# Kernel tuning notes

Hardware: AMD Instinct MI355X
Metric: run time of the kernel (lower is better)

Reference implementation:

```python
import jax, jax.numpy as jnp
import numpy as np

N = 100000
E = 1600000
IN_C, HID, OUT_C = 500, 256, 40
K, ALPHA = 10, 0.1
LN_EPS = 1e-5


def setup_inputs() -> dict:
    key = jax.random.key(0)
    ks = jax.random.split(key, 12)
    glorot = lambda k, i, o: jax.random.normal(k, (i, o), jnp.float32) * (1.0 / np.sqrt(i))
    return {
        "x": jax.random.normal(ks[0], (N, IN_C), jnp.float32),
        "edge_index": jax.random.randint(ks[1], (2, E), 0, N, jnp.int64),
        "W1": glorot(ks[2], IN_C, HID), "b1": jnp.zeros((HID,), jnp.float32),
        "g1": jnp.ones((HID,), jnp.float32), "be1": jnp.zeros((HID,), jnp.float32),
        "W2": glorot(ks[3], HID, HID), "b2": jnp.zeros((HID,), jnp.float32),
        "g2": jnp.ones((HID,), jnp.float32), "be2": jnp.zeros((HID,), jnp.float32),
        "W3": glorot(ks[4], HID, OUT_C), "b3": jnp.zeros((OUT_C,), jnp.float32),
    }


def _layernorm(h, g, b):
    mu = jnp.mean(h, axis=-1, keepdims=True)
    var = jnp.mean(jnp.square(h - mu), axis=-1, keepdims=True)
    return (h - mu) * jax.lax.rsqrt(var + LN_EPS) * g + b


def reference(x, edge_index, W1, b1, g1, be1, W2, b2, g2, be2, W3, b3):
    # --- MLP (eval mode: dropout inactive) ---
    h = _layernorm(jax.nn.gelu(x @ W1 + b1, approximate=False), g1, be1)
    h = _layernorm(jax.nn.gelu(h @ W2 + b2, approximate=False), g2, be2)
    h = h @ W3 + b3  # [N, OUT_C]

    # --- GCN normalization with self-loops (PyG gcn_norm) ---
    loops = jnp.arange(N, dtype=edge_index.dtype)
    row = jnp.concatenate([edge_index[0], loops])  # source
    col = jnp.concatenate([edge_index[1], loops])  # target
    deg = jax.ops.segment_sum(jnp.ones_like(col, jnp.float32), col, num_segments=N)
    dinv = jnp.where(deg > 0, jax.lax.rsqrt(deg), 0.0)
    norm = dinv[row] * dinv[col]  # [E+N]

    # --- APPNP: K steps of h <- (1-alpha) * A_hat h + alpha * h0 ---
    h0 = h
    for _ in range(K):
        msg = norm[:, None] * h[row]                       # gather + scale
        agg = jax.ops.segment_sum(msg, col, num_segments=N)  # scatter-add
        h = (1.0 - ALPHA) * agg + ALPHA * h0
    return h
```

## Files before the change

kernel.cpp:

```cpp
#include <hip/hip_runtime.h>
#include <hip/hip_bf16.h>
#include <math.h>

#define N_NODES 100000
#define N_EDGES 1600000
#define IN_C    500
#define HID     256
#define OUT_C   40
#define K_ITERS 10
#define ALPHA   0.1f
#define LN_EPS  1e-5f

#define K1PAD   512
#define K2PAD   256

#define SCAN_CHUNK 1024
#define NBLK_SCAN  ((N_NODES + SCAN_CHUNK - 1) / SCAN_CHUNK)

typedef __attribute__((ext_vector_type(8))) short bf16x8;
typedef __attribute__((ext_vector_type(4))) float f32x4;

__device__ __forceinline__ void split2(float a, short& hi, short& lo) {
    const unsigned ua = __float_as_uint(a);
    hi = (short)(ua >> 16);
    const float r = a - __uint_as_float(ua & 0xffff0000u);
    lo = (short)(__float_as_uint(r) >> 16);
}

__device__ __forceinline__ void async_load16(const void* g, void* l) {
    __builtin_amdgcn_global_load_lds(
        (const __attribute__((address_space(1))) void*)g,
        (__attribute__((address_space(3))) void*)l, 16, 0, 0);
}

__global__ void deg_count_kernel(const int* __restrict__ col, int* __restrict__ cnt, int e) {
    int i = blockIdx.x * blockDim.x + threadIdx.x;
    if (i < e) atomicAdd(&cnt[col[i]], 1);
}

__global__ void dinv_kernel(const int* __restrict__ cnt, float* __restrict__ dinv, int n) {
    int i = blockIdx.x * blockDim.x + threadIdx.x;
    if (i < n) dinv[i] = rsqrtf((float)cnt[i] + 1.0f);
}

__global__ __launch_bounds__(256) void scan_partial_kernel(const int* __restrict__ cnt,
                                                           int* __restrict__ bsum) {
    __shared__ int s[256];
    const int base = blockIdx.x * SCAN_CHUNK;
    const int t = threadIdx.x;
    int sum = 0;
    #pragma unroll
    for (int j = 0; j < 4; j++) {
        int idx = base + t * 4 + j;
        if (idx < N_NODES) sum += cnt[idx];
    }
    s[t] = sum;
    __syncthreads();
    for (int off = 128; off > 0; off >>= 1) {
        if (t < off) s[t] += s[t + off];
        __syncthreads();
    }
    if (t == 0) bsum[blockIdx.x] = s[0];
}

__global__ __launch_bounds__(128) void scan_bsum_kernel(int* __restrict__ bsum, int nblk) {
    __shared__ int s[128];
    const int t = threadIdx.x;
    const int orig = (t < nblk) ? bsum[t] : 0;
    s[t] = orig;
    __syncthreads();
    for (int off = 1; off < 128; off <<= 1) {
        int v = 0;
        if (t >= off) v = s[t - off];
        __syncthreads();
        s[t] += v;
        __syncthreads();
    }
    if (t < nblk) bsum[t] = s[t] - orig;
}

__global__ __launch_bounds__(256) void scan_final_kernel(const int* __restrict__ cnt,
                                                         const int* __restrict__ bsum,
                                                         int* __restrict__ offs) {
    __shared__ int s[256];
    const int base = blockIdx.x * SCAN_CHUNK;
    const int t = threadIdx.x;
    int v[4];
    int lsum = 0;
    #pragma unroll
    for (int j = 0; j < 4; j++) {
        int idx = base + t * 4 + j;
        v[j] = (idx < N_NODES) ? cnt[idx] : 0;
        lsum += v[j];
    }
    s[t] = lsum;
    __syncthreads();
    const int orig = lsum;
    for (int off = 1; off < 256; off <<= 1) {
        int u = 0;
        if (t >= off) u = s[t - off];
        __syncthreads();
        s[t] += u;
        __syncthreads();
    }
    int run = bsum[blockIdx.x] + (s[t] - orig);
    #pragma unroll
    for (int j = 0; j < 4; j++) {
        int idx = base + t * 4 + j;
        if (idx < N_NODES) offs[idx] = run;
        run += v[j];
    }
}

__global__ void set_total_kernel(int* __restrict__ offs) {
    if (threadIdx.x == 0 && blockIdx.x == 0) offs[N_NODES] = N_EDGES;
}

__global__ void csr_fill_kernel(const int* __restrict__ row, const int* __restrict__ col,
                                const float* __restrict__ dinv, const int* __restrict__ offs,
                                int* __restrict__ cursor, int2* __restrict__ csr_ew, int e) {
    int i = blockIdx.x * blockDim.x + threadIdx.x;
    if (i >= e) return;
    const int r = row[i], c = col[i];
    const int p = offs[c] + atomicAdd(&cursor[c], 1);
    csr_ew[p] = make_int2(r, __float_as_int(dinv[r] * dinv[c]));
}

__global__ __launch_bounds__(256) void wsplit_kernel(
    const float* __restrict__ W, short* __restrict__ hi, short* __restrict__ lo,
    int K, int Nn, int Kpad)
{
    const int idx = blockIdx.x * 256 + threadIdx.x;
    if (idx >= Nn * Kpad) return;
    const int n = idx / Kpad, k = idx - n * Kpad;
    const float v = (k < K) ? W[(size_t)k * Nn + n] : 0.0f;
    short h, l;
    split2(v, h, l);
    hi[idx] = h;
    lo[idx] = l;
}

#define GBM 64
#define GBN 256
#define GBK 32
#define NSTEP1 (K1PAD / GBK)
#define NSTEP2 (K2PAD / GBK)

__global__ __launch_bounds__(256, 2) void gemm1_fused_kernel(
    const float* __restrict__ X,
    const short* __restrict__ Bhi, const short* __restrict__ Blo,
    const float* __restrict__ bias, float* __restrict__ C, int M)
{
    __shared__ short As[2][2][GBM * GBK];
    __shared__ short Bs[2][2][GBN * GBK];

    const int tid  = threadIdx.x;
    const int wid  = tid >> 6, lane = tid & 63;
    const int wm   = wid >> 1, wn = wid & 1;
    const int fm   = lane & 15, fq = lane >> 4;
    const int row0 = blockIdx.x * GBM;

    const int ar   = tid >> 2;
    const int aseg = tid & 3;
    const int gr   = min(row0 + ar, M - 1);
    const int asw  = (aseg ^ ((ar >> 1) & 3)) * 8;

    f32x4 acc[2][8] = {};

    auto stageB = [&](int ks, int buf) {
        const int k0 = ks * GBK;
        #pragma unroll
        for (int i = 0; i < 4; i++) {
            const int c  = i * 256 + tid;
            const int n  = c >> 2;
            const int k8 = ((c & 3) ^ ((n >> 1) & 3)) * 8;
            const int cb = (i * 256 + wid * 64) * 8;
            const size_t oB = (size_t)n * K1PAD + k0 + k8;
            async_load16(Bhi + oB, &Bs[buf][0][cb]);
            async_load16(Blo + oB, &Bs[buf][1][cb]);
        }
    };
    auto loadX = [&](int ks, float* v) {
        const int kb = ks * GBK + aseg * 8;
        if (kb + 8 <= IN_C) {
            const float4 v0 = *(const float4*)(X + (size_t)gr * IN_C + kb);
            const float4 v1 = *(const float4*)(X + (size_t)gr * IN_C + kb + 4);
            v[0]=v0.x; v[1]=v0.y; v[2]=v0.z; v[3]=v0.w;
            v[4]=v1.x; v[5]=v1.y; v[6]=v1.z; v[7]=v1.w;
        } else {
            #pragma unroll
            for (int j = 0; j < 8; j++)
                v[j] = (kb + j < IN_C) ? X[(size_t)gr * IN_C + kb + j] : 0.0f;
        }
    };
    auto writeA = [&](const float* v, int buf) {
        bf16x8 h8, l8;
        #pragma unroll
        for (int j = 0; j < 8; j++) { short th, tl; split2(v[j], th, tl); h8[j] = th; l8[j] = tl; }
        *(bf16x8*)&As[buf][0][ar * GBK + asw] = h8;
        *(bf16x8*)&As[buf][1][ar * GBK + asw] = l8;
    };
    auto compute = [&](int buf) {
        bf16x8 ah[2], al[2];
        #pragma unroll
        for (int tm = 0; tm < 2; tm++) {
            const int r   = wm * 32 + tm * 16 + fm;
            const int ks8 = (fq ^ ((r >> 1) & 3)) * 8;
            ah[tm] = *(const bf16x8*)&As[buf][0][r * GBK + ks8];
            al[tm] = *(const bf16x8*)&As[buf][1][r * GBK + ks8];
        }
        #pragma unroll
        for (int tn = 0; tn < 8; tn++) {
            const int cc  = wn * 128 + tn * 16 + fm;
            const int ks8 = (fq ^ ((cc >> 1) & 3)) * 8;
            const bf16x8 bh = *(const bf16x8*)&Bs[buf][0][cc * GBK + ks8];
            const bf16x8 bl = *(const bf16x8*)&Bs[buf][1][cc * GBK + ks8];
            #pragma unroll
            for (int tm = 0; tm < 2; tm++) {
                acc[tm][tn] = __builtin_amdgcn_mfma_f32_16x16x32_bf16(ah[tm], bh, acc[tm][tn], 0, 0, 0);
                acc[tm][tn] = __builtin_amdgcn_mfma_f32_16x16x32_bf16(ah[tm], bl, acc[tm][tn], 0, 0, 0);
                acc[tm][tn] = __builtin_amdgcn_mfma_f32_16x16x32_bf16(al[tm], bh, acc[tm][tn], 0, 0, 0);
            }
        }
    };

    float xvA[8], xvB[8];
    loadX(0, xvA);
    stageB(0, 0);
    loadX(1, xvB);
    writeA(xvA, 0);
    __syncthreads();

    #pragma unroll
    for (int ks = 0; ks < NSTEP1; ks += 2) {
        if (ks + 1 < NSTEP1) stageB(ks + 1, 1);
        if (ks + 2 < NSTEP1) loadX(ks + 2, xvA);
        compute(0);
        if (ks + 1 < NSTEP1) writeA(xvB, 1);
        __syncthreads();
        if (ks + 1 < NSTEP1) {
            if (ks + 2 < NSTEP1) stageB(ks + 2, 0);
            if (ks + 3 < NSTEP1) loadX(ks + 3, xvB);
            compute(1);
            if (ks + 2 < NSTEP1) writeA(xvA, 0);
            __syncthreads();
        }
    }

    #pragma unroll
    for (int tm = 0; tm < 2; tm++) {
        #pragma unroll
        for (int tn = 0; tn < 8; tn++) {
            const int gc = wn * 128 + tn * 16 + fm;
            const float bv = bias[gc];
            #pragma unroll
            for (int r = 0; r < 4; r++) {
                const int gr2 = row0 + wm * 32 + tm * 16 + fq * 4 + r;
                if (gr2 < M) {
                    float v = acc[tm][tn][r] + bv;
                    v = 0.5f * v * (1.0f + erff(v * 0.70710678118654752f));
                    C[(size_t)gr2 * 256 + gc] = v;
                }
            }
        }
    }
}

__global__ __launch_bounds__(256, 2) void gemm2_kernel(
    const short* __restrict__ Ahi, const short* __restrict__ Alo,
    const short* __restrict__ Bhi, const short* __restrict__ Blo,
    const float* __restrict__ bias, float* __restrict__ C, int M)
{
    __shared__ short As[2][2][GBM * GBK];
    __shared__ short Bs[2][2][GBN * GBK];

    const int tid  = threadIdx.x;
    const int wid  = tid >> 6, lane = tid & 63;
    const int wm   = wid >> 1, wn = wid & 1;
    const int fm   = lane & 15, fq = lane >> 4;
    const int row0 = blockIdx.x * GBM;

    f32x4 acc[2][8] = {};

    auto stage = [&](int ks, int buf) {
        const int k0 = ks * GBK;
        {
            const int m  = tid >> 2;
            const int k8 = ((tid & 3) ^ ((m >> 1) & 3)) * 8;
            const int cb = (wid * 64) * 8;
            const size_t oA = (size_t)min(row0 + m, M - 1) * K2PAD + k0 + k8;
            async_load16(Ahi + oA, &As[buf][0][cb]);
            async_load16(Alo + oA, &As[buf][1][cb]);
        }
        #pragma unroll
        for (int i = 0; i < 4; i++) {
            const int c  = i * 256 + tid;
            const int n  = c >> 2;
            const int k8 = ((c & 3) ^ ((n >> 1) & 3)) * 8;
            const int cb = (i * 256 + wid * 64) * 8;
            const size_t oB = (size_t)n * K2PAD + k0 + k8;
            async_load16(Bhi + oB, &Bs[buf][0][cb]);
            async_load16(Blo + oB, &Bs[buf][1][cb]);
        }
    };
    auto compute = [&](int buf) {
        bf16x8 ah[2], al[2];
        #pragma unroll
        for (int tm = 0; tm < 2; tm++) {
            const int r   = wm * 32 + tm * 16 + fm;
            const int ks8 = (fq ^ ((r >> 1) & 3)) * 8;
            ah[tm] = *(const bf16x8*)&As[buf][0][r * GBK + ks8];
            al[tm] = *(const bf16x8*)&As[buf][1][r * GBK + ks8];
        }
        #pragma unroll
        for (int tn = 0; tn < 8; tn++) {
            const int cc  = wn * 128 + tn * 16 + fm;
            const int ks8 = (fq ^ ((cc >> 1) & 3)) * 8;
            const bf16x8 bh = *(const bf16x8*)&Bs[buf][0][cc * GBK + ks8];
            const bf16x8 bl = *(const bf16x8*)&Bs[buf][1][cc * GBK + ks8];
            #pragma unroll
            for (int tm = 0; tm < 2; tm++) {
                acc[tm][tn] = __builtin_amdgcn_mfma_f32_16x16x32_bf16(ah[tm], bh, acc[tm][tn], 0, 0, 0);
                acc[tm][tn] = __builtin_amdgcn_mfma_f32_16x16x32_bf16(ah[tm], bl, acc[tm][tn], 0, 0, 0);
                acc[tm][tn] = __builtin_amdgcn_mfma_f32_16x16x32_bf16(al[tm], bh, acc[tm][tn], 0, 0, 0);
            }
        }
    };

    stage(0, 0);
    __syncthreads();

    #pragma unroll
    for (int ks = 0; ks < NSTEP2; ks += 2) {
        if (ks + 1 < NSTEP2) stage(ks + 1, 1);
        compute(0);
        __syncthreads();
        if (ks + 1 < NSTEP2) {
            if (ks + 2 < NSTEP2) stage(ks + 2, 0);
            compute(1);
            __syncthreads();
        }
    }

    #pragma unroll
    for (int tm = 0; tm < 2; tm++) {
        #pragma unroll
        for (int tn = 0; tn < 8; tn++) {
            const int gc = wn * 128 + tn * 16 + fm;
            const float bv = bias[gc];
            #pragma unroll
            for (int r = 0; r < 4; r++) {
                const int gr2 = row0 + wm * 32 + tm * 16 + fq * 4 + r;
                if (gr2 < M) {
                    float v = acc[tm][tn][r] + bv;
                    v = 0.5f * v * (1.0f + erff(v * 0.70710678118654752f));
                    C[(size_t)gr2 * 256 + gc] = v;
                }
            }
        }
    }
}

__global__ __launch_bounds__(256) void layernorm_split_kernel(
    const float* __restrict__ h, const float* __restrict__ g, const float* __restrict__ b,
    short* __restrict__ hi, short* __restrict__ lo, int nrows)
{
    const int wave = threadIdx.x >> 6;
    const int lane = threadIdx.x & 63;
    const int row  = blockIdx.x * 4 + wave;
    if (row >= nrows) return;

    const float* p = h + (size_t)row * HID;
    float v[4];
    float s = 0.0f;
    #pragma unroll
    for (int j = 0; j < 4; j++) { v[j] = p[lane + 64 * j]; s += v[j]; }
    #pragma unroll
    for (int off = 32; off > 0; off >>= 1) s += __shfl_xor(s, off);
    const float mu = s * (1.0f / 256.0f);

    float vs = 0.0f;
    #pragma unroll
    for (int j = 0; j < 4; j++) { float d = v[j] - mu; vs += d * d; }
    #pragma unroll
    for (int off = 32; off > 0; off >>= 1) vs += __shfl_xor(vs, off);
    const float rs = rsqrtf(vs * (1.0f / 256.0f) + LN_EPS);

    #pragma unroll
    for (int j = 0; j < 4; j++) {
        const int c = lane + 64 * j;
        const float o = (v[j] - mu) * rs * g[c] + b[c];
        short th, tl;
        split2(o, th, tl);
        hi[(size_t)row * HID + c] = th;
        lo[(size_t)row * HID + c] = tl;
    }
}

__global__ __launch_bounds__(256) void ln_gemm3_kernel(
    const float* __restrict__ h, const float* __restrict__ g, const float* __restrict__ b,
    const float* __restrict__ W, const float* __restrict__ bias,
    float* __restrict__ C, int nrows)
{
    __shared__ float Ws[HID * OUT_C];
    __shared__ float bs[OUT_C];
    __shared__ float rowbuf[4][HID];

    for (int i = threadIdx.x; i < HID * OUT_C; i += 256) Ws[i] = W[i];
    if (threadIdx.x < OUT_C) bs[threadIdx.x] = bias[threadIdx.x];

    const int wave = threadIdx.x >> 6;
    const int lane = threadIdx.x & 63;
    const int row  = blockIdx.x * 4 + wave;
    const bool alive = (row < nrows);

    if (alive) {
        const float* p = h + (size_t)row * HID;
        float v[4];
        float s = 0.0f;
        #pragma unroll
        for (int j = 0; j < 4; j++) { v[j] = p[lane + 64 * j]; s += v[j]; }
        #pragma unroll
        for (int off = 32; off > 0; off >>= 1) s += __shfl_xor(s, off);
        const float mu = s * (1.0f / 256.0f);

        float vs = 0.0f;
        #pragma unroll
        for (int j = 0; j < 4; j++) { float d = v[j] - mu; vs += d * d; }
        #pragma unroll
        for (int off = 32; off > 0; off >>= 1) vs += __shfl_xor(vs, off);
        const float rs = rsqrtf(vs * (1.0f / 256.0f) + LN_EPS);

        #pragma unroll
        for (int j = 0; j < 4; j++) {
            const int c = lane + 64 * j;
            rowbuf[wave][c] = (v[j] - mu) * rs * g[c] + b[c];
        }
    }
    __syncthreads();

    if (alive && lane < OUT_C) {
        float s = 0.0f;
        #pragma unroll 8
        for (int k = 0; k < HID; k++)
            s += rowbuf[wave][k] * Ws[k * OUT_C + lane];
        C[(size_t)row * OUT_C + lane] = s + bs[lane];
    }
}

__global__ __launch_bounds__(256) void appnp_kernel(
    const int* __restrict__ offs, const int2* __restrict__ csr_ew,
    const float* __restrict__ dinv,
    const float* __restrict__ h, const float* __restrict__ h0,
    float* __restrict__ out)
{
    const int node = blockIdx.x * 4 + (threadIdx.x >> 6);
    if (node >= N_NODES) return;
    const int lane = threadIdx.x & 63;
    const int g = lane / 10;
    const int q = lane - g * 10;
    const bool act = (lane < 60);

    const int start = offs[node];
    const int end   = offs[node + 1];

    const float d = dinv[node];
    float4 hs = make_float4(0.f, 0.f, 0.f, 0.f);
    float4 h0v = make_float4(0.f, 0.f, 0.f, 0.f);
    const size_t eidx = (size_t)node * OUT_C + (lane < 10 ? lane : 0) * 4;
    if (lane < 10) {
        hs  = *(const float4*)(h + eidx);
        h0v = *(const float4*)(h0 + eidx);
    }

    float ax = 0.0f, ay = 0.0f, az = 0.0f, aw = 0.0f;
    for (int e0 = start; e0 < end; e0 += 18) {
        const int ee0 = e0 + g, ee1 = ee0 + 6, ee2 = ee0 + 12;
        const bool a0 = act && (ee0 < end);
        const bool a1 = act && (ee1 < end);
        const bool a2 = act && (ee2 < end);
        const int2 ed0 = csr_ew[a0 ? ee0 : start];
        const int2 ed1 = csr_ew[a1 ? ee1 : start];
        const int2 ed2 = csr_ew[a2 ? ee2 : start];
        const float4 v0 = *(const float4*)(h + (size_t)ed0.x * OUT_C + q * 4);
        const float4 v1 = *(const float4*)(h + (size_t)ed1.x * OUT_C + q * 4);
        const float4 v2 = *(const float4*)(h + (size_t)ed2.x * OUT_C + q * 4);
        const float w0 = a0 ? __int_as_float(ed0.y) : 0.0f;
        const float w1 = a1 ? __int_as_float(ed1.y) : 0.0f;
        const float w2 = a2 ? __int_as_float(ed2.y) : 0.0f;
        ax += w0 * v0.x + w1 * v1.x + w2 * v2.x;
        ay += w0 * v0.y + w1 * v1.y + w2 * v2.y;
        az += w0 * v0.z + w1 * v1.z + w2 * v2.z;
        aw += w0 * v0.w + w1 * v1.w + w2 * v2.w;
    }

    ax += __shfl(ax, lane + 30); ay += __shfl(ay, lane + 30);
    az += __shfl(az, lane + 30); aw += __shfl(aw, lane + 30);
    {
        const float bx = __shfl(ax, lane + 10), cx = __shfl(ax, lane + 20);
        const float by = __shfl(ay, lane + 10), cy = __shfl(ay, lane + 20);
        const float bz = __shfl(az, lane + 10), cz = __shfl(az, lane + 20);
        const float bw = __shfl(aw, lane + 10), cw = __shfl(aw, lane + 20);
        ax += bx + cx; ay += by + cy; az += bz + cz; aw += bw + cw;
    }

    if (lane < 10) {
        const float self = d * d;
        float4 o;
        o.x = (1.0f - ALPHA) * (ax + self * hs.x) + ALPHA * h0v.x;
        o.y = (1.0f - ALPHA) * (ay + self * hs.y) + ALPHA * h0v.y;
        o.z = (1.0f - ALPHA) * (az + self * hs.z) + ALPHA * h0v.z;
        o.w = (1.0f - ALPHA) * (aw + self * hs.w) + ALPHA * h0v.w;
        *(float4*)(out + eidx) = o;
    }
}

extern "C" void kernel_launch(void* const* d_in, const int* in_sizes, int n_in,
                              void* d_out, int out_size, void* d_ws, size_t ws_size,
                              hipStream_t stream) {
    const float* x   = (const float*)d_in[0];
    const int*   ei  = (const int*)d_in[1];
    const float* W1  = (const float*)d_in[2];
    const float* b1  = (const float*)d_in[3];
    const float* g1  = (const float*)d_in[4];
    const float* be1 = (const float*)d_in[5];
    const float* W2  = (const float*)d_in[6];
    const float* b2  = (const float*)d_in[7];
    const float* g2  = (const float*)d_in[8];
    const float* be2 = (const float*)d_in[9];
    const float* W3  = (const float*)d_in[10];
    const float* b3  = (const float*)d_in[11];
    float* out = (float*)d_out;

    const int* e_row = ei;
    const int* e_col = ei + N_EDGES;

    float* ws = (float*)d_ws;
    size_t off = 0;
    float* dinv = ws + off; off += N_NODES;
    int*   cnt  = (int*)(ws + off); off += N_NODES;
    int*   offs = (int*)(ws + off); off += N_NODES + 1;
    int*   bsum = (int*)(ws + off); off += 128 + 3;
    short* W1hi = (short*)(ws + off); off += 65536;
    short* W1lo = (short*)(ws + off); off += 65536;
    short* W2hi = (short*)(ws + off); off += 32768;
    short* W2lo = (short*)(ws + off); off += 32768;
    float* t1 = ws + off; off += (size_t)N_NODES * HID;
    float* t2 = t1;
    float* regA = ws + off; off += (size_t)N_NODES * HID;
    short* A2hi = (short*)regA;
    short* A2lo = A2hi + (size_t)N_NODES * HID;
    int2*  csr_ew = (int2*)regA;
    float* h0 = regA + 2 * (size_t)N_EDGES;
    float* hA = h0 + (size_t)N_NODES * OUT_C;
    float* hB = hA + (size_t)N_NODES * OUT_C;

    hipMemsetAsync(cnt, 0, N_NODES * sizeof(int), stream);
    deg_count_kernel<<<(N_EDGES + 255) / 256, 256, 0, stream>>>(e_col, cnt, N_EDGES);
    dinv_kernel<<<(N_NODES + 255) / 256, 256, 0, stream>>>(cnt, dinv, N_NODES);
    scan_partial_kernel<<<NBLK_SCAN, 256, 0, stream>>>(cnt, bsum);
    scan_bsum_kernel<<<1, 128, 0, stream>>>(bsum, NBLK_SCAN);
    scan_final_kernel<<<NBLK_SCAN, 256, 0, stream>>>(cnt, bsum, offs);
    set_total_kernel<<<1, 64, 0, stream>>>(offs);

    wsplit_kernel<<<(256 * K1PAD + 255) / 256, 256, 0, stream>>>(W1, W1hi, W1lo, IN_C, 256, K1PAD);
    wsplit_kernel<<<(256 * K2PAD + 255) / 256, 256, 0, stream>>>(W2, W2hi, W2lo, HID, 256, K2PAD);

    {
        const int nblk = (N_NODES + GBM - 1) / GBM;
        gemm1_fused_kernel<<<nblk, 256, 0, stream>>>(x, W1hi, W1lo, b1, t1, N_NODES);
        layernorm_split_kernel<<<(N_NODES + 3) / 4, 256, 0, stream>>>(t1, g1, be1, A2hi, A2lo, N_NODES);
        gemm2_kernel<<<nblk, 256, 0, stream>>>(A2hi, A2lo, W2hi, W2lo, b2, t2, N_NODES);
        ln_gemm3_kernel<<<(N_NODES + 3) / 4, 256, 0, stream>>>(t2, g2, be2, W3, b3, h0, N_NODES);
    }

    hipMemsetAsync(cnt, 0, N_NODES * sizeof(int), stream);
    csr_fill_kernel<<<(N_EDGES + 255) / 256, 256, 0, stream>>>(
        e_row, e_col, dinv, offs, cnt, csr_ew, N_EDGES);

    const float* hcur = h0;
    for (int it = 0; it < K_ITERS; it++) {
        float* tgt = (it == K_ITERS - 1) ? out : ((it & 1) ? hB : hA);
        appnp_kernel<<<(N_NODES + 3) / 4, 256, 0, stream>>>(
            offs, csr_ew, dinv, hcur, h0, tgt);
        hcur = tgt;
    }
}
```

Measured before the change: 1.552 ms.

## Fuse LayerNorm into GEMM1 epilogue and run APPNP on bf16 column slices

GEMM1 now stages its GELU output tile in shared memory and applies LayerNorm plus the hi/lo split in the epilogue, which removes the separate LayerNorm kernel and the round trip of the fp32 intermediate. The APPNP propagation is split into two passes over 20-column slices. Each pass gathers neighbour features stored as bf16 copies, which shrinks the gathered working set so it fits better in cache. CSR edge loads use nontemporal hints, and the loop-unroll pragmas were removed. The price is lower precision in the gathered messages (bf16 rounding compounds over the 10 iterations), twice the kernel launches, and re-reading the CSR once per slice.

```diff
diff --git a/kernel.cpp b/kernel.cpp
--- a/kernel.cpp
+++ b/kernel.cpp
@@ -13,6 +13,7 @@
 
 #define K1PAD   512
 #define K2PAD   256
+#define SLICE_C 20
 
 #define SCAN_CHUNK 1024
 #define NBLK_SCAN  ((N_NODES + SCAN_CHUNK - 1) / SCAN_CHUNK)
@@ -27,10 +28,27 @@
     lo = (short)(__float_as_uint(r) >> 16);
 }
 
+__device__ __forceinline__ unsigned short rtn_bf16(float f) {
+    const unsigned u = __float_as_uint(f);
+    return (unsigned short)((u + 0x7FFFu + ((u >> 16) & 1u)) >> 16);
+}
+
+__device__ __forceinline__ float bf2f(unsigned short v) {
+    return __uint_as_float(((unsigned)v) << 16);
+}
+
 __device__ __forceinline__ void async_load16(const void* g, void* l) {
     __builtin_amdgcn_global_load_lds(
         (const __attribute__((address_space(1))) void*)g,
         (__attribute__((address_space(3))) void*)l, 16, 0, 0);
+}
+
+__device__ __forceinline__ int2 ld_csr_nt(const int2* p) {
+    const long long v = __builtin_nontemporal_load((const long long*)p);
+    int2 r;
+    r.x = (int)(v & 0xffffffffLL);
+    r.y = (int)(v >> 32);
+    return r;
 }
 
 __global__ void deg_count_kernel(const int* __restrict__ col, int* __restrict__ cnt, int e) {
@@ -149,10 +167,14 @@
 __global__ __launch_bounds__(256, 2) void gemm1_fused_kernel(
     const float* __restrict__ X,
     const short* __restrict__ Bhi, const short* __restrict__ Blo,
-    const float* __restrict__ bias, float* __restrict__ C, int M)
+    const float* __restrict__ bias,
+    const float* __restrict__ gam, const float* __restrict__ bet,
+    short* __restrict__ A2hi, short* __restrict__ A2lo, int M)
 {
-    __shared__ short As[2][2][GBM * GBK];
-    __shared__ short Bs[2][2][GBN * GBK];
+    __shared__ float smemf[20480];
+    short* const Asp = (short*)smemf;
+    short* const Bsp = (short*)(smemf + 4096);
+    float* const Ct  = smemf;
 
     const int tid  = threadIdx.x;
     const int wid  = tid >> 6, lane = tid & 63;
@@ -176,8 +198,8 @@
             const int k8 = ((c & 3) ^ ((n >> 1) & 3)) * 8;
             const int cb = (i * 256 + wid * 64) * 8;
             const size_t oB = (size_t)n * K1PAD + k0 + k8;
-            async_load16(Bhi + oB, &Bs[buf][0][cb]);
-            async_load16(Blo + oB, &Bs[buf][1][cb]);
+            async_load16(Bhi + oB, Bsp + (buf * 2 + 0) * (GBN * GBK) + cb);
+            async_load16(Blo + oB, Bsp + (buf * 2 + 1) * (GBN * GBK) + cb);
         }
     };
     auto loadX = [&](int ks, float* v) {
@@ -197,8 +219,8 @@
         bf16x8 h8, l8;
         #pragma unroll
         for (int j = 0; j < 8; j++) { short th, tl; split2(v[j], th, tl); h8[j] = th; l8[j] = tl; }
-        *(bf16x8*)&As[buf][0][ar * GBK + asw] = h8;
-        *(bf16x8*)&As[buf][1][ar * GBK + asw] = l8;
+        *(bf16x8*)(Asp + (buf * 2 + 0) * (GBM * GBK) + ar * GBK + asw) = h8;
+        *(bf16x8*)(Asp + (buf * 2 + 1) * (GBM * GBK) + ar * GBK + asw) = l8;
     };
     auto compute = [&](int buf) {
         bf16x8 ah[2], al[2];
@@ -206,15 +228,15 @@
         for (int tm = 0; tm < 2; tm++) {
             const int r   = wm * 32 + tm * 16 + fm;
             const int ks8 = (fq ^ ((r >> 1) & 3)) * 8;
-            ah[tm] = *(const bf16x8*)&As[buf][0][r * GBK + ks8];
-            al[tm] = *(const bf16x8*)&As[buf][1][r * GBK + ks8];
+            ah[tm] = *(const bf16x8*)(Asp + (buf * 2 + 0) * (GBM * GBK) + r * GBK + ks8);
+            al[tm] = *(const bf16x8*)(Asp + (buf * 2 + 1) * (GBM * GBK) + r * GBK + ks8);
         }
         #pragma unroll
         for (int tn = 0; tn < 8; tn++) {
             const int cc  = wn * 128 + tn * 16 + fm;
             const int ks8 = (fq ^ ((cc >> 1) & 3)) * 8;
-            const bf16x8 bh = *(const bf16x8*)&Bs[buf][0][cc * GBK + ks8];
-            const bf16x8 bl = *(const bf16x8*)&Bs[buf][1][cc * GBK + ks8];
+            const bf16x8 bh = *(const bf16x8*)(Bsp + (buf * 2 + 0) * (GBN * GBK) + cc * GBK + ks8);
+            const bf16x8 bl = *(const bf16x8*)(Bsp + (buf * 2 + 1) * (GBN * GBK) + cc * GBK + ks8);
             #pragma unroll
             for (int tm = 0; tm < 2; tm++) {
                 acc[tm][tn] = __builtin_amdgcn_mfma_f32_16x16x32_bf16(ah[tm], bh, acc[tm][tn], 0, 0, 0);
@@ -231,7 +253,6 @@
     writeA(xvA, 0);
     __syncthreads();
 
-    #pragma unroll
     for (int ks = 0; ks < NSTEP1; ks += 2) {
         if (ks + 1 < NSTEP1) stageB(ks + 1, 1);
         if (ks + 2 < NSTEP1) loadX(ks + 2, xvA);
@@ -251,16 +272,46 @@
     for (int tm = 0; tm < 2; tm++) {
         #pragma unroll
         for (int tn = 0; tn < 8; tn++) {
-            const int gc = wn * 128 + tn * 16 + fm;
-            const float bv = bias[gc];
+            const int col = wn * 128 + tn * 16 + fm;
+            const float bv = bias[col];
             #pragma unroll
             for (int r = 0; r < 4; r++) {
-                const int gr2 = row0 + wm * 32 + tm * 16 + fq * 4 + r;
-                if (gr2 < M) {
-                    float v = acc[tm][tn][r] + bv;
-                    v = 0.5f * v * (1.0f + erff(v * 0.70710678118654752f));
-                    C[(size_t)gr2 * 256 + gc] = v;
-                }
+                const int row = wm * 32 + tm * 16 + fq * 4 + r;
+                float v = acc[tm][tn][r] + bv;
+                v = 0.5f * v * (1.0f + erff(v * 0.70710678118654752f));
+                Ct[row * HID + col] = v;
+            }
+        }
+    }
+    __syncthreads();
+
+    for (int rr = 0; rr < 16; rr++) {
+        const int row = wid * 16 + rr;
+        float v[4];
+        float s = 0.0f;
+        #pragma unroll
+        for (int j = 0; j < 4; j++) { v[j] = Ct[row * HID + lane + 64 * j]; s += v[j]; }
+        #pragma unroll
+        for (int off2 = 32; off2 > 0; off2 >>= 1) s += __shfl_xor(s, off2);
+        const float mu = s * (1.0f / 256.0f);
+
+        float vs = 0.0f;
+        #pragma unroll
+        for (int j = 0; j < 4; j++) { float dd = v[j] - mu; vs += dd * dd; }
+        #pragma unroll
+        for (int off2 = 32; off2 > 0; off2 >>= 1) vs += __shfl_xor(vs, off2);
+        const float rs = rsqrtf(vs * (1.0f / 256.0f) + LN_EPS);
+
+        const int grow = row0 + row;
+        if (grow < M) {
+            #pragma unroll
+            for (int j = 0; j < 4; j++) {
+                const int c = lane + 64 * j;
+                const float o = (v[j] - mu) * rs * gam[c] + bet[c];
+                short th, tl;
+                split2(o, th, tl);
+                A2hi[(size_t)grow * HID + c] = th;
+                A2lo[(size_t)grow * HID + c] = tl;
             }
         }
     }
@@ -330,7 +381,6 @@
     stage(0, 0);
     __syncthreads();
 
-    #pragma unroll
     for (int ks = 0; ks < NSTEP2; ks += 2) {
         if (ks + 1 < NSTEP2) stage(ks + 1, 1);
         compute(0);
@@ -361,46 +411,11 @@
     }
 }
 
-__global__ __launch_bounds__(256) void layernorm_split_kernel(
-    const float* __restrict__ h, const float* __restrict__ g, const float* __restrict__ b,
-    short* __restrict__ hi, short* __restrict__ lo, int nrows)
-{
-    const int wave = threadIdx.x >> 6;
-    const int lane = threadIdx.x & 63;
-    const int row  = blockIdx.x * 4 + wave;
-    if (row >= nrows) return;
-
-    const float* p = h + (size_t)row * HID;
-    float v[4];
-    float s = 0.0f;
-    #pragma unroll
-    for (int j = 0; j < 4; j++) { v[j] = p[lane + 64 * j]; s += v[j]; }
-    #pragma unroll
-    for (int off = 32; off > 0; off >>= 1) s += __shfl_xor(s, off);
-    const float mu = s * (1.0f / 256.0f);
-
-    float vs = 0.0f;
-    #pragma unroll
-    for (int j = 0; j < 4; j++) { float d = v[j] - mu; vs += d * d; }
-    #pragma unroll
-    for (int off = 32; off > 0; off >>= 1) vs += __shfl_xor(vs, off);
-    const float rs = rsqrtf(vs * (1.0f / 256.0f) + LN_EPS);
-
-    #pragma unroll
-    for (int j = 0; j < 4; j++) {
-        const int c = lane + 64 * j;
-        const float o = (v[j] - mu) * rs * g[c] + b[c];
-        short th, tl;
-        split2(o, th, tl);
-        hi[(size_t)row * HID + c] = th;
-        lo[(size_t)row * HID + c] = tl;
-    }
-}
-
 __global__ __launch_bounds__(256) void ln_gemm3_kernel(
     const float* __restrict__ h, const float* __restrict__ g, const float* __restrict__ b,
     const float* __restrict__ W, const float* __restrict__ bias,
-    float* __restrict__ C, int nrows)
+    float* __restrict__ C, unsigned short* __restrict__ s0,
+    unsigned short* __restrict__ s1, int nrows)
 {
     __shared__ float Ws[HID * OUT_C];
     __shared__ float bs[OUT_C];
@@ -444,15 +459,19 @@
         #pragma unroll 8
         for (int k = 0; k < HID; k++)
             s += rowbuf[wave][k] * Ws[k * OUT_C + lane];
-        C[(size_t)row * OUT_C + lane] = s + bs[lane];
-    }
-}
-
-__global__ __launch_bounds__(256) void appnp_kernel(
+        const float o = s + bs[lane];
+        C[(size_t)row * OUT_C + lane] = o;
+        if (lane < SLICE_C) s0[(size_t)row * SLICE_C + lane] = rtn_bf16(o);
+        else                s1[(size_t)row * SLICE_C + lane - SLICE_C] = rtn_bf16(o);
+    }
+}
+
+__global__ __launch_bounds__(256) void appnp_slice_kernel(
     const int* __restrict__ offs, const int2* __restrict__ csr_ew,
     const float* __restrict__ dinv,
-    const float* __restrict__ h, const float* __restrict__ h0,
-    float* __restrict__ out)
+    const float* __restrict__ h, const unsigned short* __restrict__ hbp,
+    const float* __restrict__ h0,
+    float* __restrict__ out, unsigned short* __restrict__ outb, int p)
 {
     const int node = blockIdx.x * 4 + (threadIdx.x >> 6);
     if (node >= N_NODES) return;
@@ -465,53 +484,52 @@
     const int end   = offs[node + 1];
 
     const float d = dinv[node];
-    float4 hs = make_float4(0.f, 0.f, 0.f, 0.f);
-    float4 h0v = make_float4(0.f, 0.f, 0.f, 0.f);
-    const size_t eidx = (size_t)node * OUT_C + (lane < 10 ? lane : 0) * 4;
+    float2 hs  = make_float2(0.f, 0.f);
+    float2 h0v = make_float2(0.f, 0.f);
+    const size_t fbase = (size_t)node * OUT_C + p * SLICE_C + (lane < 10 ? lane : 0) * 2;
     if (lane < 10) {
-        hs  = *(const float4*)(h + eidx);
-        h0v = *(const float4*)(h0 + eidx);
-    }
-
-    float ax = 0.0f, ay = 0.0f, az = 0.0f, aw = 0.0f;
+        hs  = *(const float2*)(h + fbase);
+        h0v = *(const float2*)(h0 + fbase);
+    }
+
+    float ax = 0.0f, ay = 0.0f;
     for (int e0 = start; e0 < end; e0 += 18) {
         const int ee0 = e0 + g, ee1 = ee0 + 6, ee2 = ee0 + 12;
         const bool a0 = act && (ee0 < end);
         const bool a1 = act && (ee1 < end);
         const bool a2 = act && (ee2 < end);
-        const int2 ed0 = csr_ew[a0 ? ee0 : start];
-        const int2 ed1 = csr_ew[a1 ? ee1 : start];
-        const int2 ed2 = csr_ew[a2 ? ee2 : start];
-        const float4 v0 = *(const float4*)(h + (size_t)ed0.x * OUT_C + q * 4);
-        const float4 v1 = *(const float4*)(h + (size_t)ed1.x * OUT_C + q * 4);
-        const float4 v2 = *(const float4*)(h + (size_t)ed2.x * OUT_C + q * 4);
+        const int2 ed0 = ld_csr_nt(&csr_ew[a0 ? ee0 : start]);
+        const int2 ed1 = ld_csr_nt(&csr_ew[a1 ? ee1 : start]);
+        const int2 ed2 = ld_csr_nt(&csr_ew[a2 ? ee2 : start]);
+        const unsigned u0 = *(const unsigned*)(hbp + (size_t)ed0.x * SLICE_C + q * 2);
+        const unsigned u1 = *(const unsigned*)(hbp + (size_t)ed1.x * SLICE_C + q * 2);
+        const unsigned u2 = *(const unsigned*)(hbp + (size_t)ed2.x * SLICE_C + q * 2);
         const float w0 = a0 ? __int_as_float(ed0.y) : 0.0f;
         const float w1 = a1 ? __int_as_float(ed1.y) : 0.0f;
         const float w2 = a2 ? __int_as_float(ed2.y) : 0.0f;
-        ax += w0 * v0.x + w1 * v1.x + w2 * v2.x;
-        ay += w0 * v0.y + w1 * v1.y + w2 * v2.y;
-        az += w0 * v0.z + w1 * v1.z + w2 * v2.z;
-        aw += w0 * v0.w + w1 * v1.w + w2 * v2.w;
+        ax += w0 * bf2f((unsigned short)(u0 & 0xffff))
+            + w1 * bf2f((unsigned short)(u1 & 0xffff))
+            + w2 * bf2f((unsigned short)(u2 & 0xffff));
+        ay += w0 * bf2f((unsigned short)(u0 >> 16))
+            + w1 * bf2f((unsigned short)(u1 >> 16))
+            + w2 * bf2f((unsigned short)(u2 >> 16));
     }
 
     ax += __shfl(ax, lane + 30); ay += __shfl(ay, lane + 30);
-    az += __shfl(az, lane + 30); aw += __shfl(aw, lane + 30);
     {
         const float bx = __shfl(ax, lane + 10), cx = __shfl(ax, lane + 20);
         const float by = __shfl(ay, lane + 10), cy = __shfl(ay, lane + 20);
-        const float bz = __shfl(az, lane + 10), cz = __shfl(az, lane + 20);
-        const float bw = __shfl(aw, lane + 10), cw = __shfl(aw, lane + 20);
-        ax += bx + cx; ay += by + cy; az += bz + cz; aw += bw + cw;
+        ax += bx + cx; ay += by + cy;
     }
 
     if (lane < 10) {
         const float self = d * d;
-        float4 o;
+        float2 o;
         o.x = (1.0f - ALPHA) * (ax + self * hs.x) + ALPHA * h0v.x;
         o.y = (1.0f - ALPHA) * (ay + self * hs.y) + ALPHA * h0v.y;
-        o.z = (1.0f - ALPHA) * (az + self * hs.z) + ALPHA * h0v.z;
-        o.w = (1.0f - ALPHA) * (aw + self * hs.w) + ALPHA * h0v.w;
-        *(float4*)(out + eidx) = o;
+        *(float2*)(out + fbase) = o;
+        const unsigned packed = (unsigned)rtn_bf16(o.x) | ((unsigned)rtn_bf16(o.y) << 16);
+        *(unsigned*)(outb + (size_t)node * SLICE_C + lane * 2) = packed;
     }
 }
 
@@ -545,8 +563,7 @@
     short* W1lo = (short*)(ws + off); off += 65536;
     short* W2hi = (short*)(ws + off); off += 32768;
     short* W2lo = (short*)(ws + off); off += 32768;
-    float* t1 = ws + off; off += (size_t)N_NODES * HID;
-    float* t2 = t1;
+    float* t2 = ws + off; off += (size_t)N_NODES * HID;
     float* regA = ws + off; off += (size_t)N_NODES * HID;
     short* A2hi = (short*)regA;
     short* A2lo = A2hi + (size_t)N_NODES * HID;
@@ -554,6 +571,12 @@
     float* h0 = regA + 2 * (size_t)N_EDGES;
     float* hA = h0 + (size_t)N_NODES * OUT_C;
     float* hB = hA + (size_t)N_NODES * OUT_C;
+    unsigned short* h0s0 = (unsigned short*)(hB + (size_t)N_NODES * OUT_C);
+    unsigned short* h0s1 = h0s0 + (size_t)N_NODES * SLICE_C;
+    unsigned short* hAs0 = h0s1 + (size_t)N_NODES * SLICE_C;
+    unsigned short* hAs1 = hAs0 + (size_t)N_NODES * SLICE_C;
+    unsigned short* hBs0 = hAs1 + (size_t)N_NODES * SLICE_C;
+    unsigned short* hBs1 = hBs0 + (size_t)N_NODES * SLICE_C;
 
     hipMemsetAsync(cnt, 0, N_NODES * sizeof(int), stream);
     deg_count_kernel<<<(N_EDGES + 255) / 256, 256, 0, stream>>>(e_col, cnt, N_EDGES);
@@ -568,10 +591,9 @@
 
     {
         const int nblk = (N_NODES + GBM - 1) / GBM;
-        gemm1_fused_kernel<<<nblk, 256, 0, stream>>>(x, W1hi, W1lo, b1, t1, N_NODES);
-        layernorm_split_kernel<<<(N_NODES + 3) / 4, 256, 0, stream>>>(t1, g1, be1, A2hi, A2lo, N_NODES);
+        gemm1_fused_kernel<<<nblk, 256, 0, stream>>>(x, W1hi, W1lo, b1, g1, be1, A2hi, A2lo, N_NODES);
         gemm2_kernel<<<nblk, 256, 0, stream>>>(A2hi, A2lo, W2hi, W2lo, b2, t2, N_NODES);
-        ln_gemm3_kernel<<<(N_NODES + 3) / 4, 256, 0, stream>>>(t2, g2, be2, W3, b3, h0, N_NODES);
+        ln_gemm3_kernel<<<(N_NODES + 3) / 4, 256, 0, stream>>>(t2, g2, be2, W3, b3, h0, h0s0, h0s1, N_NODES);
     }
 
     hipMemsetAsync(cnt, 0, N_NODES * sizeof(int), stream);
@@ -579,10 +601,18 @@
         e_row, e_col, dinv, offs, cnt, csr_ew, N_EDGES);
 
     const float* hcur = h0;
+    const unsigned short* hcs0 = h0s0;
+    const unsigned short* hcs1 = h0s1;
     for (int it = 0; it < K_ITERS; it++) {
         float* tgt = (it == K_ITERS - 1) ? out : ((it & 1) ? hB : hA);
-        appnp_kernel<<<(N_NODES + 3) / 4, 256, 0, stream>>>(
-            offs, csr_ew, dinv, hcur, h0, tgt);
+        unsigned short* ts0 = (it & 1) ? hBs0 : hAs0;
+        unsigned short* ts1 = (it & 1) ? hBs1 : hAs1;
+        appnp_slice_kernel<<<(N_NODES + 3) / 4, 256, 0, stream>>>(
+            offs, csr_ew, dinv, hcur, hcs0, h0, tgt, ts0, 0);
+        appnp_slice_kernel<<<(N_NODES + 3) / 4, 256, 0, stream>>>(
+            offs, csr_ew, dinv, hcur, hcs1, h0, tgt, ts1, 1);
         hcur = tgt;
-    }
-}
+        hcs0 = ts0;
+        hcs1 = ts1;
+    }
+}
```

After: 1.819 ms. +17.2%, slower.
